# Kernel optimization log

Hardware: AMD Instinct MI355X
Metric: run time of the kernel (lower is better)

Reference implementation:

```python
import jax, jax.numpy as jnp
import numpy as np


def eops_2_to_2(x):
    # x: (N, D, m, m) -> (N, D, 15, m, m), Maron et al. equivariant basis with 'inf' normalization
    m = x.shape[-1]
    fm = float(m)
    eye = jnp.eye(m, dtype=x.dtype)
    diag = jnp.diagonal(x, axis1=-2, axis2=-1)          # (N, D, m)
    sum_diag = diag.sum(-1, keepdims=True)              # (N, D, 1)
    sum_rows = x.sum(-1)                                # (N, D, m) sum over columns j
    sum_cols = x.sum(-2)                                # (N, D, m) sum over rows i
    tot = x.sum((-2, -1))                               # (N, D)

    de = lambda v: v[..., :, None] * eye                # diag_embed (N,D,m) -> (N,D,m,m)
    b_row = lambda v: jnp.broadcast_to(v[..., :, None], v.shape + (m,))           # row i constant = v[i]
    b_col = lambda v: jnp.broadcast_to(v[..., None, :], v.shape[:-1] + (m, m))    # col j constant = v[j]

    op1 = de(diag)
    op2 = de(jnp.broadcast_to(sum_diag, diag.shape)) / fm
    op3 = de(sum_rows) / fm
    op4 = de(sum_cols) / fm
    op5 = de(jnp.broadcast_to(tot[..., None], diag.shape)) / (fm * fm)
    op6 = b_row(sum_cols) / fm
    op7 = b_row(sum_rows) / fm
    op8 = b_col(sum_cols) / fm
    op9 = b_col(sum_rows) / fm
    op10 = x
    op11 = jnp.swapaxes(x, -1, -2)
    op12 = b_row(diag)
    op13 = b_col(diag)
    op14 = jnp.broadcast_to(sum_diag[..., None], x.shape) / fm
    op15 = jnp.broadcast_to(tot[..., None, None], x.shape) / (fm * fm)
    return jnp.stack([op1, op2, op3, op4, op5, op6, op7, op8,
                      op9, op10, op11, op12, op13, op14, op15], axis=2)


def setup_inputs() -> dict:
    key = jax.random.key(0)
    k1, k2 = jax.random.split(key)
    N, D, S, B, m = 32, 32, 32, 15, 128
    std = np.sqrt(2.0 / (D + S + B)).astype(np.float32)
    inputs = jax.random.normal(k1, (N, D, m, m), dtype=jnp.float32)
    coefs = jax.random.normal(k2, (D, S, B), dtype=jnp.float32) * std
    bias = jnp.zeros((1, S, 1, 1), dtype=jnp.float32)
    diag_bias = jnp.zeros((1, S, 1, 1), dtype=jnp.float32)
    return {"inputs": inputs, "coefs": coefs, "bias": bias, "diag_bias": diag_bias}


def reference(inputs, coefs, bias, diag_bias):
    ops = eops_2_to_2(inputs)                               # (N, D, 15, m, m)
    out = jnp.einsum('dsb,ndbij->nsij', coefs, ops)         # (N, S, m, m)
    m = out.shape[-1]
    eye = jnp.eye(m, dtype=out.dtype)[None, None]           # (1,1,m,m)
    return out + bias + eye * diag_bias
```

## Files before the change

kernel.cpp:

```cpp
#include <hip/hip_runtime.h>

#define N_ 32
#define D_ 32
#define S_ 32
#define M_ 128
#define MM_ (M_ * M_)
#define INV_M (1.0f / 128.0f)
#define INV_M2 (1.0f / (128.0f * 128.0f))

typedef float f32x4 __attribute__((ext_vector_type(4)));
typedef __bf16 bf16x8 __attribute__((ext_vector_type(8)));

#define WS_ROWSUM  0
#define WS_COLSUM  131072
#define WS_DIAG    262144
#define WS_SUMDIAG 393216
#define WS_TOT     394240
#define WS_RV      395264
#define WS_CV      526336
#define WS_DG      657408
#define WS_WBF16   788480
#define WS_X16     789760

__device__ __forceinline__ unsigned short f2bf(float f) {
    unsigned u = __float_as_uint(f);
    u += 0x7fffu + ((u >> 16) & 1u);
    return (unsigned short)(u >> 16);
}

__device__ __forceinline__ void decode_pair(int b, int& AR, int& AC, int& BR, int& BC, int& diagpair) {
    if (b < 28) {
        int ti = 0, rem = b;
        while (rem >= 7 - ti) { rem -= 7 - ti; ++ti; }
        int tj = ti + 1 + rem;
        AR = ti * 16; AC = tj * 16;
        BR = tj * 16; BC = ti * 16;
        diagpair = 0;
    } else {
        int p = b - 28;
        AR = AC = (2 * p) * 16;
        BR = BC = (2 * p + 1) * 16;
        diagpair = 1;
    }
}

__global__ __launch_bounds__(256) void eq2_reduce(const float* __restrict__ x,
                                                  float* __restrict__ ws) {
    int nd = blockIdx.x;
    int t  = threadIdx.x;
    int g  = t >> 5;
    int j4 = t & 31;

    const float4* xp = (const float4*)(x + (size_t)nd * MM_);
    unsigned short* x16 = (unsigned short*)(ws + WS_X16) + (size_t)nd * MM_;

    float* rowsum  = ws + WS_ROWSUM;
    float* colsum  = ws + WS_COLSUM;
    float* diag    = ws + WS_DIAG;
    float* sumdiag = ws + WS_SUMDIAG;
    float* tot     = ws + WS_TOT;

    float4 cs = {0.f, 0.f, 0.f, 0.f};
    float dsum = 0.f, ttot = 0.f;

    for (int r = 0; r < 16; ++r) {
        int i = g * 16 + r;
        float4 v = xp[i * 32 + j4];
        cs.x += v.x; cs.y += v.y; cs.z += v.z; cs.w += v.w;
        float rp = v.x + v.y + v.z + v.w;
        ttot += rp;
        {
            uint2 pk;
            pk.x = (unsigned)f2bf(v.x) | ((unsigned)f2bf(v.y) << 16);
            pk.y = (unsigned)f2bf(v.z) | ((unsigned)f2bf(v.w) << 16);
            *(uint2*)(x16 + i * M_ + 4 * j4) = pk;
        }
        int c = i - 4 * j4;
        if (c >= 0 && c < 4) {
            float dv = (c == 0) ? v.x : (c == 1) ? v.y : (c == 2) ? v.z : v.w;
            diag[nd * M_ + i] = dv;
            dsum += dv;
        }
        float rs = rp;
        for (int msk = 1; msk < 32; msk <<= 1) rs += __shfl_xor(rs, msk, 64);
        if ((t & 31) == 0) rowsum[nd * M_ + i] = rs;
    }

    __shared__ float4 cs_lds[8][32];
    __shared__ float  red[2][4];
    cs_lds[g][j4] = cs;

    for (int msk = 1; msk < 64; msk <<= 1) {
        dsum += __shfl_xor(dsum, msk, 64);
        ttot += __shfl_xor(ttot, msk, 64);
    }
    int wave = t >> 6, lane = t & 63;
    if (lane == 0) { red[0][wave] = dsum; red[1][wave] = ttot; }
    __syncthreads();

    if (t < 32) {
        float4 a = cs_lds[0][t];
        for (int gg = 1; gg < 8; ++gg) {
            float4 b = cs_lds[gg][t];
            a.x += b.x; a.y += b.y; a.z += b.z; a.w += b.w;
        }
        ((float4*)(colsum + nd * M_))[t] = a;
    }
    if (t == 0) {
        sumdiag[nd] = red[0][0] + red[0][1] + red[0][2] + red[0][3];
        tot[nd]     = red[1][0] + red[1][1] + red[1][2] + red[1][3];
    }
}

__global__ __launch_bounds__(128) void eq2_combine(const float* __restrict__ coefs,
                                                   const float* __restrict__ bias,
                                                   const float* __restrict__ diag_bias,
                                                   float* __restrict__ ws) {
    int b = blockIdx.x;
    int n = b >> 5, s = b & 31;
    int i = threadIdx.x;

    const float* rowsum  = ws + WS_ROWSUM;
    const float* colsum  = ws + WS_COLSUM;
    const float* diag    = ws + WS_DIAG;
    const float* sumdiag = ws + WS_SUMDIAG;
    const float* tot     = ws + WS_TOT;

    float rv = 0.f, cv = 0.f, dg = 0.f, kk = 0.f;
    for (int d = 0; d < D_; ++d) {
        const float* cf = coefs + (d * S_ + s) * 15;
        float rs = rowsum[(n * D_ + d) * M_ + i];
        float c2 = colsum[(n * D_ + d) * M_ + i];
        float dv = diag[(n * D_ + d) * M_ + i];
        float sd = sumdiag[n * D_ + d];
        float tt = tot[n * D_ + d];
        rv += (cf[5] * c2 + cf[6] * rs) * INV_M + cf[11] * dv;
        cv += (cf[7] * c2 + cf[8] * rs) * INV_M + cf[12] * dv;
        dg += cf[0] * dv + (cf[1] * sd + cf[2] * rs + cf[3] * c2) * INV_M
              + cf[4] * tt * INV_M2;
        kk += cf[13] * sd * INV_M + cf[14] * tt * INV_M2;
    }
    ws[WS_RV + (n * S_ + s) * M_ + i] = rv + kk + bias[s];
    ws[WS_CV + (n * S_ + s) * M_ + i] = cv;
    ws[WS_DG + (n * S_ + s) * M_ + i] = dg + diag_bias[s];

    if (n == 0 && i < 32) {
        int d = i;
        unsigned short* wsbf = (unsigned short*)(ws + WS_WBF16);
        const float* cf = coefs + (d * S_ + s) * 15;
        wsbf[s * 40 + d]        = f2bf(cf[9]);
        wsbf[(32 + s) * 40 + d] = f2bf(cf[10]);
    }
}

__global__ __launch_bounds__(512, 4) void eq2_main(const float* __restrict__ ws_,
                                                   float* __restrict__ out) {
    const float* ws = (const float*)__builtin_assume_aligned(ws_, 256);
    int lid = blockIdx.x;
    int n   = (lid & 7) + 8 * (lid >> 8);
    int b   = (lid >> 3) & 31;

    int AR, AC, BR, BC, diagpair;
    decode_pair(b, AR, AC, BR, BC, diagpair);

    int t    = threadIdx.x;
    int w    = t >> 6;
    int lane = t & 63;
    int lg   = lane >> 4;
    int lj   = lane & 15;

    __shared__ float trf[8 * 545];
    __shared__ float lds_rv[S_][32];
    __shared__ float lds_cv[S_][32];
    __shared__ float lds_dg[S_][32];

    const unsigned short* wsbf = (const unsigned short*)(ws + WS_WBF16);
    const unsigned short* x16n = (const unsigned short*)(ws + WS_X16) + (size_t)n * D_ * MM_;

    bf16x8 A10[2], A11[2];
#pragma unroll
    for (int mt = 0; mt < 2; ++mt) {
        A10[mt] = *(const bf16x8*)(wsbf + (mt * 16 + lj) * 40 + lg * 8);
        A11[mt] = *(const bf16x8*)(wsbf + (32 + mt * 16 + lj) * 40 + lg * 8);
    }

    {
        const float* Rv = ws + WS_RV;
        const float* Cv = ws + WS_CV;
        const float* Dg = ws + WS_DG;
#pragma unroll
        for (int k = 0; k < 2; ++k) {
            int idx = k * 512 + t;
            int s = idx >> 5, q = idx & 31;
            int base = (n * S_ + s) * M_;
            int ro = (q < 16) ? AR + q : BR + (q - 16);
            int co = (q < 16) ? AC + q : BC + (q - 16);
            lds_rv[s][q] = Rv[base + ro];
            lds_cv[s][q] = Cv[base + co];
            if (diagpair) lds_dg[s][q] = Dg[base + ro];
        }
    }

    f32x4 aY[4][2], aZ[4][2];
#pragma unroll
    for (int k = 0; k < 4; ++k)
#pragma unroll
        for (int mt = 0; mt < 2; ++mt) { aY[k][mt] = 0.f; aZ[k][mt] = 0.f; }

#pragma unroll
    for (int half = 0; half < 2; ++half) {
        unsigned short uv[2][8];
#pragma unroll
        for (int kk = 0; kk < 2; ++kk) {
            int k  = half * 2 + kk;
            int nt = w * 4 + k;
            int tt = nt >> 4, il = nt & 15;
            int Rt = tt ? BR : AR, Ct = tt ? BC : AC;
            const unsigned short* src = x16n + (Rt + il) * M_ + Ct + lj + (size_t)(lg * 8) * MM_;
#pragma unroll
            for (int e = 0; e < 8; ++e)
                uv[kk][e] = src[(size_t)e * MM_];
        }
#pragma unroll
        for (int kk = 0; kk < 2; ++kk) {
            int k = half * 2 + kk;
            union { unsigned uu[4]; bf16x8 v; } cvt;
#pragma unroll
            for (int e = 0; e < 4; ++e)
                cvt.uu[e] = (unsigned)uv[kk][2 * e] | ((unsigned)uv[kk][2 * e + 1] << 16);
            bf16x8 Bf = cvt.v;
            aY[k][0] = __builtin_amdgcn_mfma_f32_16x16x32_bf16(A10[0], Bf, aY[k][0], 0, 0, 0);
            aY[k][1] = __builtin_amdgcn_mfma_f32_16x16x32_bf16(A10[1], Bf, aY[k][1], 0, 0, 0);
            aZ[k][0] = __builtin_amdgcn_mfma_f32_16x16x32_bf16(A11[0], Bf, aZ[k][0], 0, 0, 0);
            aZ[k][1] = __builtin_amdgcn_mfma_f32_16x16x32_bf16(A11[1], Bf, aZ[k][1], 0, 0, 0);
        }
    }

#pragma unroll
    for (int r = 0; r < 4; ++r) {
        if (r) __syncthreads();
#pragma unroll
        for (int k = 0; k < 4; ++k) {
            int nt = w * 4 + k;
            int tt = nt >> 4, il = nt & 15;
#pragma unroll
            for (int mt = 0; mt < 2; ++mt)
                trf[(mt * 4 + lg) * 545 + tt * 272 + il * 17 + lj] = aZ[k][mt][r];
        }
        __syncthreads();
#pragma unroll
        for (int k = 0; k < 4; ++k) {
            int nt = w * 4 + k;
            int tt = nt >> 4, il = nt & 15;
            int ttp = diagpair ? tt : 1 - tt;
            int Rt = tt ? BR : AR, Ct = tt ? BC : AC;
#pragma unroll
            for (int mt = 0; mt < 2; ++mt) {
                int s = mt * 16 + 4 * lg + r;
                float zt = trf[(mt * 4 + lg) * 545 + ttp * 272 + lj * 17 + il];
                float o = aY[k][mt][r] + zt + lds_rv[s][tt * 16 + il] + lds_cv[s][tt * 16 + lj];
                if (diagpair && il == lj) o += lds_dg[s][tt * 16 + il];
                out[(size_t)(n * S_ + s) * MM_ + (Rt + il) * M_ + Ct + lj] = o;
            }
        }
    }
}

extern "C" void kernel_launch(void* const* d_in, const int* in_sizes, int n_in,
                              void* d_out, int out_size, void* d_ws, size_t ws_size,
                              hipStream_t stream) {
    const float* x         = (const float*)d_in[0];
    const float* coefs     = (const float*)d_in[1];
    const float* bias      = (const float*)d_in[2];
    const float* diag_bias = (const float*)d_in[3];
    float* out = (float*)d_out;
    float* ws  = (float*)d_ws;

    hipLaunchKernelGGL(eq2_reduce,  dim3(N_ * D_), dim3(256), 0, stream, x, ws);
    hipLaunchKernelGGL(eq2_combine, dim3(N_ * S_), dim3(128), 0, stream, coefs, bias, diag_bias, ws);
    hipLaunchKernelGGL(eq2_main,    dim3(1024), dim3(512), 0, stream, ws, out);
}
```

Baseline: 53.09 us.

## Process two tile pairs per block with prefetch and restructure reduce via LDS

The main kernel now launches half as many blocks, each handling two tile pairs, and prefetches the first half of the second pair's bf16 gather before running the first pair's epilogue, so global-load latency overlaps with the LDS transpose and stores. The reduce kernel replaces per-row shuffle reductions with LDS staging of partial row sums, then computes row sums, total and diagonal sum from shared memory. The cost is higher register pressure from the extra prefetch buffers, fewer blocks to fill the GPU, and more barriers in the reduce kernel.

```diff
diff --git a/kernel.cpp b/kernel.cpp
--- a/kernel.cpp
+++ b/kernel.cpp
@@ -54,21 +54,17 @@
     const float4* xp = (const float4*)(x + (size_t)nd * MM_);
     unsigned short* x16 = (unsigned short*)(ws + WS_X16) + (size_t)nd * MM_;
 
-    float* rowsum  = ws + WS_ROWSUM;
-    float* colsum  = ws + WS_COLSUM;
-    float* diag    = ws + WS_DIAG;
-    float* sumdiag = ws + WS_SUMDIAG;
-    float* tot     = ws + WS_TOT;
+    __shared__ float  rp[128][33];
+    __shared__ float4 csl[8][32];
+    __shared__ float  dgl[128];
 
     float4 cs = {0.f, 0.f, 0.f, 0.f};
-    float dsum = 0.f, ttot = 0.f;
 
     for (int r = 0; r < 16; ++r) {
         int i = g * 16 + r;
         float4 v = xp[i * 32 + j4];
         cs.x += v.x; cs.y += v.y; cs.z += v.z; cs.w += v.w;
-        float rp = v.x + v.y + v.z + v.w;
-        ttot += rp;
+        rp[i][j4] = v.x + v.y + v.z + v.w;
         {
             uint2 pk;
             pk.x = (unsigned)f2bf(v.x) | ((unsigned)f2bf(v.y) << 16);
@@ -78,37 +74,40 @@
         int c = i - 4 * j4;
         if (c >= 0 && c < 4) {
             float dv = (c == 0) ? v.x : (c == 1) ? v.y : (c == 2) ? v.z : v.w;
-            diag[nd * M_ + i] = dv;
-            dsum += dv;
-        }
-        float rs = rp;
-        for (int msk = 1; msk < 32; msk <<= 1) rs += __shfl_xor(rs, msk, 64);
-        if ((t & 31) == 0) rowsum[nd * M_ + i] = rs;
-    }
-
-    __shared__ float4 cs_lds[8][32];
-    __shared__ float  red[2][4];
-    cs_lds[g][j4] = cs;
-
-    for (int msk = 1; msk < 64; msk <<= 1) {
-        dsum += __shfl_xor(dsum, msk, 64);
-        ttot += __shfl_xor(ttot, msk, 64);
-    }
-    int wave = t >> 6, lane = t & 63;
-    if (lane == 0) { red[0][wave] = dsum; red[1][wave] = ttot; }
+            (ws + WS_DIAG)[nd * M_ + i] = dv;
+            dgl[i] = dv;
+        }
+    }
+    csl[g][j4] = cs;
     __syncthreads();
 
     if (t < 32) {
-        float4 a = cs_lds[0][t];
+        float4 a = csl[0][t];
         for (int gg = 1; gg < 8; ++gg) {
-            float4 b = cs_lds[gg][t];
+            float4 b = csl[gg][t];
             a.x += b.x; a.y += b.y; a.z += b.z; a.w += b.w;
         }
-        ((float4*)(colsum + nd * M_))[t] = a;
-    }
-    if (t == 0) {
-        sumdiag[nd] = red[0][0] + red[0][1] + red[0][2] + red[0][3];
-        tot[nd]     = red[1][0] + red[1][1] + red[1][2] + red[1][3];
+        ((float4*)((ws + WS_COLSUM) + nd * M_))[t] = a;
+    }
+    if (t < 128) {
+        float rs = 0.f;
+#pragma unroll
+        for (int k = 0; k < 32; ++k) rs += rp[t][k];
+        (ws + WS_ROWSUM)[nd * M_ + t] = rs;
+        rp[t][32] = rs;
+    }
+    __syncthreads();
+    if (t < 64) {
+        float tt = rp[t][32] + rp[t + 64][32];
+        float sd = dgl[t] + dgl[t + 64];
+        for (int m = 1; m < 64; m <<= 1) {
+            tt += __shfl_xor(tt, m, 64);
+            sd += __shfl_xor(sd, m, 64);
+        }
+        if (t == 0) {
+            (ws + WS_TOT)[nd]     = tt;
+            (ws + WS_SUMDIAG)[nd] = sd;
+        }
     }
 }
 
@@ -156,12 +155,11 @@
 __global__ __launch_bounds__(512, 4) void eq2_main(const float* __restrict__ ws_,
                                                    float* __restrict__ out) {
     const float* ws = (const float*)__builtin_assume_aligned(ws_, 256);
-    int lid = blockIdx.x;
-    int n   = (lid & 7) + 8 * (lid >> 8);
-    int b   = (lid >> 3) & 31;
-
-    int AR, AC, BR, BC, diagpair;
-    decode_pair(b, AR, AC, BR, BC, diagpair);
+    int lid  = blockIdx.x;
+    int xcd  = lid & 7;
+    int u    = lid >> 3;
+    int n    = xcd + 8 * (u >> 4);
+    int sub  = u & 15;
 
     int t    = threadIdx.x;
     int w    = t >> 6;
@@ -184,7 +182,7 @@
         A11[mt] = *(const bf16x8*)(wsbf + (32 + mt * 16 + lj) * 40 + lg * 8);
     }
 
-    {
+    auto stage_rv = [&](int AR, int AC, int BR, int BC, int dp) {
         const float* Rv = ws + WS_RV;
         const float* Cv = ws + WS_CV;
         const float* Dg = ws + WS_DG;
@@ -197,22 +195,13 @@
             int co = (q < 16) ? AC + q : BC + (q - 16);
             lds_rv[s][q] = Rv[base + ro];
             lds_cv[s][q] = Cv[base + co];
-            if (diagpair) lds_dg[s][q] = Dg[base + ro];
-        }
-    }
-
-    f32x4 aY[4][2], aZ[4][2];
-#pragma unroll
-    for (int k = 0; k < 4; ++k)
-#pragma unroll
-        for (int mt = 0; mt < 2; ++mt) { aY[k][mt] = 0.f; aZ[k][mt] = 0.f; }
-
-#pragma unroll
-    for (int half = 0; half < 2; ++half) {
-        unsigned short uv[2][8];
+            if (dp) lds_dg[s][q] = Dg[base + ro];
+        }
+    };
+    auto gather2 = [&](int AR, int AC, int BR, int BC, int kbase, unsigned short uv[2][8]) {
 #pragma unroll
         for (int kk = 0; kk < 2; ++kk) {
-            int k  = half * 2 + kk;
+            int k  = kbase + kk;
             int nt = w * 4 + k;
             int tt = nt >> 4, il = nt & 15;
             int Rt = tt ? BR : AR, Ct = tt ? BC : AC;
@@ -221,9 +210,11 @@
             for (int e = 0; e < 8; ++e)
                 uv[kk][e] = src[(size_t)e * MM_];
         }
+    };
+    auto mfma2 = [&](unsigned short uv[2][8], int kbase, f32x4 aY[4][2], f32x4 aZ[4][2]) {
 #pragma unroll
         for (int kk = 0; kk < 2; ++kk) {
-            int k = half * 2 + kk;
+            int k = kbase + kk;
             union { unsigned uu[4]; bf16x8 v; } cvt;
 #pragma unroll
             for (int e = 0; e < 4; ++e)
@@ -234,36 +225,77 @@
             aZ[k][0] = __builtin_amdgcn_mfma_f32_16x16x32_bf16(A11[0], Bf, aZ[k][0], 0, 0, 0);
             aZ[k][1] = __builtin_amdgcn_mfma_f32_16x16x32_bf16(A11[1], Bf, aZ[k][1], 0, 0, 0);
         }
-    }
-
-#pragma unroll
-    for (int r = 0; r < 4; ++r) {
-        if (r) __syncthreads();
-#pragma unroll
-        for (int k = 0; k < 4; ++k) {
-            int nt = w * 4 + k;
-            int tt = nt >> 4, il = nt & 15;
-#pragma unroll
-            for (int mt = 0; mt < 2; ++mt)
-                trf[(mt * 4 + lg) * 545 + tt * 272 + il * 17 + lj] = aZ[k][mt][r];
-        }
-        __syncthreads();
-#pragma unroll
-        for (int k = 0; k < 4; ++k) {
-            int nt = w * 4 + k;
-            int tt = nt >> 4, il = nt & 15;
-            int ttp = diagpair ? tt : 1 - tt;
-            int Rt = tt ? BR : AR, Ct = tt ? BC : AC;
-#pragma unroll
-            for (int mt = 0; mt < 2; ++mt) {
-                int s = mt * 16 + 4 * lg + r;
-                float zt = trf[(mt * 4 + lg) * 545 + ttp * 272 + lj * 17 + il];
-                float o = aY[k][mt][r] + zt + lds_rv[s][tt * 16 + il] + lds_cv[s][tt * 16 + lj];
-                if (diagpair && il == lj) o += lds_dg[s][tt * 16 + il];
-                out[(size_t)(n * S_ + s) * MM_ + (Rt + il) * M_ + Ct + lj] = o;
+    };
+    auto epilogue = [&](int AR, int AC, int BR, int BC, int dp,
+                        f32x4 aY[4][2], f32x4 aZ[4][2]) {
+#pragma unroll
+        for (int r = 0; r < 4; ++r) {
+            if (r) __syncthreads();
+#pragma unroll
+            for (int k = 0; k < 4; ++k) {
+                int nt = w * 4 + k;
+                int tt = nt >> 4, il = nt & 15;
+#pragma unroll
+                for (int mt = 0; mt < 2; ++mt)
+                    trf[(mt * 4 + lg) * 545 + tt * 272 + il * 17 + lj] = aZ[k][mt][r];
             }
-        }
-    }
+            __syncthreads();
+#pragma unroll
+            for (int k = 0; k < 4; ++k) {
+                int nt = w * 4 + k;
+                int tt = nt >> 4, il = nt & 15;
+                int ttp = dp ? tt : 1 - tt;
+                int Rt = tt ? BR : AR, Ct = tt ? BC : AC;
+#pragma unroll
+                for (int mt = 0; mt < 2; ++mt) {
+                    int s = mt * 16 + 4 * lg + r;
+                    float zt = trf[(mt * 4 + lg) * 545 + ttp * 272 + lj * 17 + il];
+                    float o = aY[k][mt][r] + zt + lds_rv[s][tt * 16 + il] + lds_cv[s][tt * 16 + lj];
+                    if (dp && il == lj) o += lds_dg[s][tt * 16 + il];
+                    out[(size_t)(n * S_ + s) * MM_ + (Rt + il) * M_ + Ct + lj] = o;
+                }
+            }
+        }
+    };
+
+    int AR0, AC0, BR0, BC0, dp0, AR1, AC1, BR1, BC1, dp1;
+    decode_pair(2 * sub,     AR0, AC0, BR0, BC0, dp0);
+    decode_pair(2 * sub + 1, AR1, AC1, BR1, BC1, dp1);
+
+    f32x4 aY[4][2], aZ[4][2];
+#pragma unroll
+    for (int k = 0; k < 4; ++k)
+#pragma unroll
+        for (int mt = 0; mt < 2; ++mt) { aY[k][mt] = 0.f; aZ[k][mt] = 0.f; }
+
+    stage_rv(AR0, AC0, BR0, BC0, dp0);
+    {
+        unsigned short uva[2][8], uvb[2][8];
+        gather2(AR0, AC0, BR0, BC0, 0, uva);
+        gather2(AR0, AC0, BR0, BC0, 2, uvb);
+        mfma2(uva, 0, aY, aZ);
+        mfma2(uvb, 2, aY, aZ);
+    }
+    unsigned short uv1a[2][8];
+    gather2(AR1, AC1, BR1, BC1, 0, uv1a);
+
+    __syncthreads();
+    epilogue(AR0, AC0, BR0, BC0, dp0, aY, aZ);
+    __syncthreads();
+
+    stage_rv(AR1, AC1, BR1, BC1, dp1);
+    {
+        unsigned short uv1b[2][8];
+        gather2(AR1, AC1, BR1, BC1, 2, uv1b);
+#pragma unroll
+        for (int k = 0; k < 4; ++k)
+#pragma unroll
+            for (int mt = 0; mt < 2; ++mt) { aY[k][mt] = 0.f; aZ[k][mt] = 0.f; }
+        mfma2(uv1a, 0, aY, aZ);
+        mfma2(uv1b, 2, aY, aZ);
+    }
+    __syncthreads();
+    epilogue(AR1, AC1, BR1, BC1, dp1, aY, aZ);
 }
 
 extern "C" void kernel_launch(void* const* d_in, const int* in_sizes, int n_in,
@@ -278,5 +310,5 @@
 
     hipLaunchKernelGGL(eq2_reduce,  dim3(N_ * D_), dim3(256), 0, stream, x, ws);
     hipLaunchKernelGGL(eq2_combine, dim3(N_ * S_), dim3(128), 0, stream, coefs, bias, diag_bias, ws);
-    hipLaunchKernelGGL(eq2_main,    dim3(1024), dim3(512), 0, stream, ws, out);
-}
+    hipLaunchKernelGGL(eq2_main,    dim3(512), dim3(512), 0, stream, ws, out);
+}
```

Measured after the change: 61.02 us. 1.15x slower.
